# Kernel tuning notes

Hardware: AMD Instinct MI355X
Metric: run time of the kernel (lower is better)

The kernel has to match this reference:

```python
import math
import jax, jax.numpy as jnp
import numpy as np

B, S, HID = 1, 2048, 4096
NH, NKV, HD = 32, 8, 128          # query heads, kv heads, head dim (HID // NH)
G, R = NKV, NH // NKV             # kv groups, query heads per kv group
Q_SIZE, KV_SIZE = NH * HD, NKV * HD


def _get_alibi_slopes(n_heads):
    n = 2 ** math.floor(math.log2(n_heads))
    m0 = 2.0 ** (-8.0 / n)
    slopes = np.power(m0, np.arange(1, n + 1))
    if n < n_heads:
        m1 = 2.0 ** (-4.0 / n)
        mm = np.power(m1, np.arange(1, 1 + 2 * (n_heads - n), 2))
        slopes = np.concatenate([slopes, mm])
    return slopes  # NTK ratio 1.0 -> identity


def setup_inputs() -> dict:
    key = jax.random.key(0)
    k1, k2, k3 = jax.random.split(key, 3)
    positions = jnp.broadcast_to(jnp.arange(S, dtype=jnp.int32), (B, S))
    hidden_states = jax.random.normal(k1, (B, S, HID), dtype=jnp.float32)
    wqkv = jax.random.normal(k2, (Q_SIZE + 2 * KV_SIZE, HID), dtype=jnp.float32) * 0.02
    wo = jax.random.normal(k3, (HID, Q_SIZE), dtype=jnp.float32) * 0.02
    return {"positions": positions, "hidden_states": hidden_states,
            "wqkv": wqkv, "wo": wo}


def reference(positions, hidden_states, wqkv, wo):
    scale = HD ** -0.5
    slopes = jnp.asarray(_get_alibi_slopes(NH), dtype=hidden_states.dtype).reshape(G, R)

    # fused QKV projection (no bias)
    qkv = jnp.einsum('bsh,oh->bso', hidden_states, wqkv)
    q = qkv[..., :Q_SIZE].reshape(B, S, G, R, HD)
    k = qkv[..., Q_SIZE:Q_SIZE + KV_SIZE].reshape(B, S, G, HD)
    v = qkv[..., Q_SIZE + KV_SIZE:].reshape(B, S, G, HD)

    # GQA attention scores: [B, G, R, Sq, Sk]
    scores = jnp.einsum('bqgrd,bkgd->bgrqk', q, k) * scale

    # sqrt-ALiBi bias: -slope * sqrt(q_pos - k_pos), causal mask where k_pos > q_pos
    dist = positions[:, :, None] - positions[:, None, :]            # [B, Sq, Sk]
    bias = -slopes[None, :, :, None, None] * jnp.sqrt(
        jnp.maximum(dist, 0).astype(scores.dtype))[:, None, None]
    neg_inf = jnp.asarray(jnp.finfo(scores.dtype).min, scores.dtype)
    scores = jnp.where(dist[:, None, None] < 0, neg_inf, scores + bias)

    attn = jax.nn.softmax(scores, axis=-1)
    out = jnp.einsum('bgrqk,bkgd->bqgrd', attn, v).reshape(B, S, Q_SIZE)
    return jnp.einsum('bso,ho->bsh', out, wo)
```

## Files before the change

kernel.cpp:

```cpp
#include <hip/hip_runtime.h>
#include <stdint.h>

typedef __attribute__((ext_vector_type(8))) short short8;
typedef __attribute__((ext_vector_type(4))) float floatx4;

#define S_LEN 2048
#define OTOT  6144
#define KOFF  4096
#define VOFF  5120

__device__ __forceinline__ unsigned short f2bf(float f) {
  unsigned int u = __float_as_uint(f);
  u += 0x7FFFu + ((u >> 16) & 1u);
  return (unsigned short)(u >> 16);
}

__device__ __forceinline__ void gload_lds16(const void* g, void* l) {
  __builtin_amdgcn_global_load_lds(
      (const __attribute__((address_space(1))) void*)g,
      (__attribute__((address_space(3))) void*)l, 16, 0, 0);
}

__global__ void cast_bf16_kernel(const float* __restrict__ in,
                                 unsigned short* __restrict__ out, int n4) {
  int i = blockIdx.x * blockDim.x + threadIdx.x;
  int stride = gridDim.x * blockDim.x;
  for (; i < n4; i += stride) {
    float4 v = ((const float4*)in)[i];
    ushort4 o;
    o.x = f2bf(v.x); o.y = f2bf(v.y); o.z = f2bf(v.z); o.w = f2bf(v.w);
    ((ushort4*)out)[i] = o;
  }
}

__global__ void transpose_v_kernel(const unsigned short* __restrict__ qkv,
                                   unsigned short* __restrict__ vt) {
  int tid = blockIdx.x * 256 + threadIdx.x;
  int gd = tid >> 8;
  int s8 = (tid & 255) << 3;
  short8 v;
#pragma unroll
  for (int j = 0; j < 8; ++j)
    v[j] = (short)qkv[(size_t)(s8 + j) * OTOT + VOFF + gd];
  *(short8*)&vt[(size_t)gd * S_LEN + s8] = v;
}

template <typename CT>
__global__ __launch_bounds__(256, 2) void gemm_bt_kernel(
    const unsigned short* __restrict__ A, const unsigned short* __restrict__ B,
    CT* __restrict__ C, int M, int N, int K) {
  __shared__ unsigned short As[128 * 64];
  __shared__ unsigned short Bs[128 * 64];

  int nbn = N >> 7;
  int nwg = gridDim.x;
  int bid = blockIdx.x;
  if ((nwg & 7) == 0) bid = (bid & 7) * (nwg >> 3) + (bid >> 3);
  int bm = bid / nbn, bn = bid % nbn;

  int tid = threadIdx.x;
  int lane = tid & 63, wave = tid >> 6;
  int lr = lane & 15, lh = lane >> 4;
  int wm = (wave >> 1) << 6, wn = (wave & 1) << 6;

  floatx4 acc[4][4];
#pragma unroll
  for (int i = 0; i < 4; ++i)
#pragma unroll
    for (int j = 0; j < 4; ++j) acc[i][j] = (floatx4){0.f, 0.f, 0.f, 0.f};

  const size_t arow = (size_t)bm * 128;
  const size_t brow = (size_t)bn * 128;
  int nk = K >> 6;
  for (int kt = 0; kt < nk; ++kt) {
#pragma unroll
    for (int i = 0; i < 4; ++i) {
      int lin = i * 4096 + tid * 16;
      int row = lin >> 7;
      int colb = (lin & 127) ^ ((row & 7) << 4);
      gload_lds16(&A[(arow + row) * K + kt * 64 + (colb >> 1)],
                  &As[(i * 4096 + wave * 1024) >> 1]);
    }
#pragma unroll
    for (int i = 0; i < 4; ++i) {
      int lin = i * 4096 + tid * 16;
      int row = lin >> 7;
      int colb = (lin & 127) ^ ((row & 7) << 4);
      gload_lds16(&B[(brow + row) * K + kt * 64 + (colb >> 1)],
                  &Bs[(i * 4096 + wave * 1024) >> 1]);
    }
    __syncthreads();
#pragma unroll
    for (int kk = 0; kk < 2; ++kk) {
      short8 af[4], bfr[4];
#pragma unroll
      for (int mi = 0; mi < 4; ++mi) {
        int row = wm + mi * 16 + lr;
        int off = (row << 7) | ((kk * 64 + lh * 16) ^ ((row & 7) << 4));
        af[mi] = *(const short8*)&As[off >> 1];
      }
#pragma unroll
      for (int ni = 0; ni < 4; ++ni) {
        int row = wn + ni * 16 + lr;
        int off = (row << 7) | ((kk * 64 + lh * 16) ^ ((row & 7) << 4));
        bfr[ni] = *(const short8*)&Bs[off >> 1];
      }
#pragma unroll
      for (int mi = 0; mi < 4; ++mi)
#pragma unroll
        for (int ni = 0; ni < 4; ++ni)
          acc[mi][ni] = __builtin_amdgcn_mfma_f32_16x16x32_bf16(
              af[mi], bfr[ni], acc[mi][ni], 0, 0, 0);
    }
    __syncthreads();
  }
#pragma unroll
  for (int mi = 0; mi < 4; ++mi)
#pragma unroll
    for (int ni = 0; ni < 4; ++ni)
#pragma unroll
      for (int r = 0; r < 4; ++r) {
        size_t grow = arow + wm + mi * 16 + lh * 4 + r;
        size_t gcol = brow + wn + ni * 16 + lr;
        float v = acc[mi][ni][r];
        if constexpr (sizeof(CT) == 2)
          ((unsigned short*)C)[grow * N + gcol] = f2bf(v);
        else
          C[grow * N + gcol] = v;
      }
}

__global__ __launch_bounds__(256, 2) void attn_kernel(
    const unsigned short* __restrict__ qkv, const unsigned short* __restrict__ vt,
    const int* __restrict__ pos, unsigned short* __restrict__ aout) {
  __shared__ unsigned short Klds[64 * 128];
  __shared__ unsigned short Vlds[128 * 64];
  __shared__ unsigned short Plds[4][16 * 72];

  int bid = blockIdx.x;
  bid = (bid & 7) * 128 + (bid >> 3);
  int h = bid >> 5, qt = bid & 31;
  int g = h >> 2;
  float slope = exp2f(-0.25f * (float)(h + 1));

  int tid = threadIdx.x, lane = tid & 63, wave = tid >> 6;
  int lr = lane & 15, lh = lane >> 4;
  int qbase = qt * 64;
  int qrow0 = qbase + wave * 16;

  short8 aq[4];
#pragma unroll
  for (int kk = 0; kk < 4; ++kk)
    aq[kk] = *(const short8*)&qkv[(size_t)(qrow0 + lr) * OTOT + h * 128 + kk * 32 + lh * 8];

  int qpos[4];
#pragma unroll
  for (int r = 0; r < 4; ++r) qpos[r] = pos[qrow0 + lh * 4 + r];

  float m_run[4] = {-3.0e38f, -3.0e38f, -3.0e38f, -3.0e38f};
  float l_run[4] = {0.f, 0.f, 0.f, 0.f};
  floatx4 acc_o[8];
#pragma unroll
  for (int n = 0; n < 8; ++n) acc_o[n] = (floatx4){0.f, 0.f, 0.f, 0.f};

  const float scale = 0.08838834764831845f;
  const float LOG2E = 1.4426950408889634f;

  for (int j = 0; j <= qt; ++j) {
    int kbase = j * 64;
#pragma unroll
    for (int i = 0; i < 4; ++i) {
      int lin = i * 4096 + tid * 16;
      int row = lin >> 8;
      int colb = (lin & 255) ^ ((row & 7) << 4);
      gload_lds16(&qkv[(size_t)(kbase + row) * OTOT + KOFF + g * 128 + (colb >> 1)],
                  &Klds[(i * 4096 + wave * 1024) >> 1]);
    }
#pragma unroll
    for (int i = 0; i < 4; ++i) {
      int lin = i * 4096 + tid * 16;
      int row = lin >> 7;
      int colb = (lin & 127) ^ ((row & 7) << 4);
      gload_lds16(&vt[(size_t)(g * 128 + row) * S_LEN + kbase + (colb >> 1)],
                  &Vlds[(i * 4096 + wave * 1024) >> 1]);
    }
    __syncthreads();

    floatx4 sc[4];
#pragma unroll
    for (int n = 0; n < 4; ++n) sc[n] = (floatx4){0.f, 0.f, 0.f, 0.f};
#pragma unroll
    for (int kk = 0; kk < 4; ++kk)
#pragma unroll
      for (int n = 0; n < 4; ++n) {
        int row = n * 16 + lr;
        int off = (row << 8) | ((kk * 64 + lh * 16) ^ ((row & 7) << 4));
        short8 bk = *(const short8*)&Klds[off >> 1];
        sc[n] = __builtin_amdgcn_mfma_f32_16x16x32_bf16(aq[kk], bk, sc[n], 0, 0, 0);
      }

    float p[4][4];
#pragma unroll
    for (int n = 0; n < 4; ++n) {
      int kp = pos[kbase + n * 16 + lr];
#pragma unroll
      for (int r = 0; r < 4; ++r) {
        int dist = qpos[r] - kp;
        p[n][r] = (dist < 0) ? -3.0e38f
                             : sc[n][r] * scale - slope * sqrtf((float)dist);
      }
    }
#pragma unroll
    for (int r = 0; r < 4; ++r) {
      float mx = fmaxf(fmaxf(p[0][r], p[1][r]), fmaxf(p[2][r], p[3][r]));
      mx = fmaxf(mx, __shfl_xor(mx, 1));
      mx = fmaxf(mx, __shfl_xor(mx, 2));
      mx = fmaxf(mx, __shfl_xor(mx, 4));
      mx = fmaxf(mx, __shfl_xor(mx, 8));
      float mnew = fmaxf(m_run[r], mx);
      float rs = 0.f;
#pragma unroll
      for (int n = 0; n < 4; ++n) {
        float e = exp2f((p[n][r] - mnew) * LOG2E);
        p[n][r] = e;
        rs += e;
      }
      rs += __shfl_xor(rs, 1);
      rs += __shfl_xor(rs, 2);
      rs += __shfl_xor(rs, 4);
      rs += __shfl_xor(rs, 8);
      float alpha = exp2f((m_run[r] - mnew) * LOG2E);
      l_run[r] = l_run[r] * alpha + rs;
      m_run[r] = mnew;
#pragma unroll
      for (int n = 0; n < 8; ++n) acc_o[n][r] *= alpha;
    }
#pragma unroll
    for (int n = 0; n < 4; ++n)
#pragma unroll
      for (int r = 0; r < 4; ++r)
        Plds[wave][(lh * 4 + r) * 72 + n * 16 + lr] = f2bf(p[n][r]);

#pragma unroll
    for (int kk = 0; kk < 2; ++kk) {
      short8 pa = *(const short8*)&Plds[wave][lr * 72 + kk * 32 + lh * 8];
#pragma unroll
      for (int n = 0; n < 8; ++n) {
        int row = n * 16 + lr;
        int off = (row << 7) | ((kk * 64 + lh * 16) ^ ((row & 7) << 4));
        short8 bv = *(const short8*)&Vlds[off >> 1];
        acc_o[n] = __builtin_amdgcn_mfma_f32_16x16x32_bf16(pa, bv, acc_o[n], 0, 0, 0);
      }
    }
    __syncthreads();
  }

#pragma unroll
  for (int r = 0; r < 4; ++r) {
    float inv = 1.0f / l_run[r];
    size_t grow = (size_t)(qrow0 + lh * 4 + r);
#pragma unroll
    for (int n = 0; n < 8; ++n)
      aout[grow * 4096 + h * 128 + n * 16 + lr] = f2bf(acc_o[n][r] * inv);
  }
}

extern "C" void kernel_launch(void* const* d_in, const int* in_sizes, int n_in,
                              void* d_out, int out_size, void* d_ws, size_t ws_size,
                              hipStream_t stream) {
  (void)in_sizes; (void)n_in; (void)out_size;
  const int* positions = (const int*)d_in[0];
  const float* hidden = (const float*)d_in[1];
  const float* wqkv = (const float*)d_in[2];
  const float* wo = (const float*)d_in[3];
  float* out = (float*)d_out;

  char* w = (char*)d_ws;
  unsigned short* hbf   = (unsigned short*)(w);
  unsigned short* wqbf  = (unsigned short*)(w + 16777216);
  unsigned short* wobf  = (unsigned short*)(w + 67108864);
  unsigned short* qkv   = (unsigned short*)(w + 100663296);
  unsigned short* vtb   = (unsigned short*)(w + 125829120);
  unsigned short* attnb = (unsigned short*)(w + 130023424);
  if (ws_size < 146800640) return;

  cast_bf16_kernel<<<2048, 256, 0, stream>>>(hidden, hbf, 2048 * 4096 / 4);
  cast_bf16_kernel<<<2048, 256, 0, stream>>>(wqkv, wqbf, 6144 * 4096 / 4);
  cast_bf16_kernel<<<2048, 256, 0, stream>>>(wo, wobf, 4096 * 4096 / 4);

  gemm_bt_kernel<unsigned short><<<768, 256, 0, stream>>>(hbf, wqbf, qkv, 2048, 6144, 4096);
  transpose_v_kernel<<<1024, 256, 0, stream>>>(qkv, vtb);
  attn_kernel<<<1024, 256, 0, stream>>>(qkv, vtb, positions, attnb);
  gemm_bt_kernel<float><<<512, 256, 0, stream>>>(attnb, wobf, out, 2048, 4096, 4096);
}
```

Before: 629.1 us.

## Restructure attention to transposed S^T layout keeping P in registers, tile V transpose

The attention kernel now computes S transposed (K as the A operand, Q as B), so each lane owns one query row. Softmax probabilities can then be packed straight into MFMA operands with v_cvt_pk_bf16_f32, with no LDS round trip, and row reductions need only two cross-lane shuffles. It also adds lazy rescaling, which skips the accumulator update unless the max grows past a threshold. Other changes: pre-scaling by log2e, heaviest query tiles scheduled first, occupancy hint raised to 4, and an LDS-tiled V transpose with coalesced accesses. The risks are register pressure at the higher occupancy target and small numeric drift from the deferred rescale.

```diff
diff --git a/kernel.cpp b/kernel.cpp
--- a/kernel.cpp
+++ b/kernel.cpp
@@ -13,6 +13,12 @@
   unsigned int u = __float_as_uint(f);
   u += 0x7FFFu + ((u >> 16) & 1u);
   return (unsigned short)(u >> 16);
+}
+
+__device__ __forceinline__ unsigned int pack2bf(float lo, float hi) {
+  unsigned int r;
+  asm("v_cvt_pk_bf16_f32 %0, %1, %2" : "=v"(r) : "v"(lo), "v"(hi));
+  return r;
 }
 
 __device__ __forceinline__ void gload_lds16(const void* g, void* l) {
@@ -33,16 +39,30 @@
   }
 }
 
-__global__ void transpose_v_kernel(const unsigned short* __restrict__ qkv,
-                                   unsigned short* __restrict__ vt) {
-  int tid = blockIdx.x * 256 + threadIdx.x;
-  int gd = tid >> 8;
-  int s8 = (tid & 255) << 3;
-  short8 v;
-#pragma unroll
-  for (int j = 0; j < 8; ++j)
-    v[j] = (short)qkv[(size_t)(s8 + j) * OTOT + VOFF + gd];
-  *(short8*)&vt[(size_t)gd * S_LEN + s8] = v;
+__global__ __launch_bounds__(256) void transpose_v_kernel(
+    const unsigned short* __restrict__ qkv, unsigned short* __restrict__ vt) {
+  __shared__ unsigned short T[128 * 74];
+  int s0 = (blockIdx.x & 31) * 64;
+  int g = blockIdx.x >> 5;
+  int tid = threadIdx.x;
+#pragma unroll
+  for (int it = 0; it < 16; ++it) {
+    int idx = it * 256 + tid;
+    int srow = idx >> 6;
+    int dc = idx & 63;
+    unsigned int v = *(const unsigned int*)&qkv[(size_t)(s0 + srow) * OTOT + VOFF + g * 128 + dc * 2];
+    T[(2 * dc) * 74 + srow] = (unsigned short)(v & 0xFFFF);
+    T[(2 * dc + 1) * 74 + srow] = (unsigned short)(v >> 16);
+  }
+  __syncthreads();
+#pragma unroll
+  for (int it = 0; it < 16; ++it) {
+    int odx = it * 256 + tid;
+    int d = odx >> 5;
+    int sc2 = odx & 31;
+    unsigned int w = *(const unsigned int*)&T[d * 74 + 2 * sc2];
+    *(unsigned int*)&vt[(size_t)(g * 128 + d) * S_LEN + s0 + 2 * sc2] = w;
+  }
 }
 
 template <typename CT>
@@ -130,49 +150,44 @@
       }
 }
 
-__global__ __launch_bounds__(256, 2) void attn_kernel(
+__global__ __launch_bounds__(256, 4) void attn_kernel(
     const unsigned short* __restrict__ qkv, const unsigned short* __restrict__ vt,
     const int* __restrict__ pos, unsigned short* __restrict__ aout) {
   __shared__ unsigned short Klds[64 * 128];
   __shared__ unsigned short Vlds[128 * 64];
-  __shared__ unsigned short Plds[4][16 * 72];
 
   int bid = blockIdx.x;
-  bid = (bid & 7) * 128 + (bid >> 3);
-  int h = bid >> 5, qt = bid & 31;
+  int h = bid & 31;
+  int qt = 31 - (bid >> 5);
   int g = h >> 2;
-  float slope = exp2f(-0.25f * (float)(h + 1));
+  const float L2E = 1.4426950408889634f;
+  float slope2 = exp2f(-0.25f * (float)(h + 1)) * L2E;
+  const float QS2 = 0.08838834764831845f * L2E;
+  const float THR = 8.0f * L2E;
 
   int tid = threadIdx.x, lane = tid & 63, wave = tid >> 6;
   int lr = lane & 15, lh = lane >> 4;
-  int qbase = qt * 64;
-  int qrow0 = qbase + wave * 16;
-
-  short8 aq[4];
+  int qrow0 = qt * 64 + wave * 16;
+
+  short8 qf[4];
 #pragma unroll
   for (int kk = 0; kk < 4; ++kk)
-    aq[kk] = *(const short8*)&qkv[(size_t)(qrow0 + lr) * OTOT + h * 128 + kk * 32 + lh * 8];
-
-  int qpos[4];
-#pragma unroll
-  for (int r = 0; r < 4; ++r) qpos[r] = pos[qrow0 + lh * 4 + r];
-
-  float m_run[4] = {-3.0e38f, -3.0e38f, -3.0e38f, -3.0e38f};
-  float l_run[4] = {0.f, 0.f, 0.f, 0.f};
-  floatx4 acc_o[8];
-#pragma unroll
-  for (int n = 0; n < 8; ++n) acc_o[n] = (floatx4){0.f, 0.f, 0.f, 0.f};
-
-  const float scale = 0.08838834764831845f;
-  const float LOG2E = 1.4426950408889634f;
-
-  for (int j = 0; j <= qt; ++j) {
+    qf[kk] = *(const short8*)&qkv[(size_t)(qrow0 + lr) * OTOT + h * 128 + kk * 32 + lh * 8];
+  int qpos = pos[qrow0 + lr];
+
+  float m_run = -3.0e38f, l_run = 0.f;
+  floatx4 acc[8];
+#pragma unroll
+  for (int n = 0; n < 8; ++n) acc[n] = (floatx4){0.f, 0.f, 0.f, 0.f};
+
+  for (int jj = 0; jj <= qt; ++jj) {
+    int j = qt - jj;
     int kbase = j * 64;
 #pragma unroll
     for (int i = 0; i < 4; ++i) {
       int lin = i * 4096 + tid * 16;
       int row = lin >> 8;
-      int colb = (lin & 255) ^ ((row & 7) << 4);
+      int colb = (lin & 255) ^ (((row >> 1) & 7) << 4);
       gload_lds16(&qkv[(size_t)(kbase + row) * OTOT + KOFF + g * 128 + (colb >> 1)],
                   &Klds[(i * 4096 + wave * 1024) >> 1]);
     }
@@ -190,78 +205,88 @@
 #pragma unroll
     for (int n = 0; n < 4; ++n) sc[n] = (floatx4){0.f, 0.f, 0.f, 0.f};
 #pragma unroll
-    for (int kk = 0; kk < 4; ++kk)
-#pragma unroll
-      for (int n = 0; n < 4; ++n) {
-        int row = n * 16 + lr;
-        int off = (row << 8) | ((kk * 64 + lh * 16) ^ ((row & 7) << 4));
-        short8 bk = *(const short8*)&Klds[off >> 1];
-        sc[n] = __builtin_amdgcn_mfma_f32_16x16x32_bf16(aq[kk], bk, sc[n], 0, 0, 0);
-      }
-
-    float p[4][4];
-#pragma unroll
     for (int n = 0; n < 4; ++n) {
-      int kp = pos[kbase + n * 16 + lr];
+      int rowk = 32 * (n & 1) + 2 * lr + (n >> 1);
+      int swz = ((rowk >> 1) & 7) << 4;
+#pragma unroll
+      for (int kk = 0; kk < 4; ++kk) {
+        short8 kf = *(const short8*)&Klds[((rowk << 8) | ((kk * 64 + lh * 16) ^ swz)) >> 1];
+        sc[n] = __builtin_amdgcn_mfma_f32_16x16x32_bf16(kf, qf[kk], sc[n], 0, 0, 0);
+      }
+    }
+
+    int4 a0 = *(const int4*)&pos[kbase + lh * 8];
+    int4 a1 = *(const int4*)&pos[kbase + lh * 8 + 4];
+    int4 b0 = *(const int4*)&pos[kbase + 32 + lh * 8];
+    int4 b1 = *(const int4*)&pos[kbase + 32 + lh * 8 + 4];
+    int klo[8] = {a0.x, a0.y, a0.z, a0.w, a1.x, a1.y, a1.z, a1.w};
+    int khi[8] = {b0.x, b0.y, b0.z, b0.w, b1.x, b1.y, b1.z, b1.w};
+
+#pragma unroll
+    for (int n = 0; n < 4; ++n)
 #pragma unroll
       for (int r = 0; r < 4; ++r) {
-        int dist = qpos[r] - kp;
-        p[n][r] = (dist < 0) ? -3.0e38f
-                             : sc[n][r] * scale - slope * sqrtf((float)dist);
-      }
-    }
-#pragma unroll
-    for (int r = 0; r < 4; ++r) {
-      float mx = fmaxf(fmaxf(p[0][r], p[1][r]), fmaxf(p[2][r], p[3][r]));
-      mx = fmaxf(mx, __shfl_xor(mx, 1));
-      mx = fmaxf(mx, __shfl_xor(mx, 2));
-      mx = fmaxf(mx, __shfl_xor(mx, 4));
-      mx = fmaxf(mx, __shfl_xor(mx, 8));
-      float mnew = fmaxf(m_run[r], mx);
-      float rs = 0.f;
-#pragma unroll
-      for (int n = 0; n < 4; ++n) {
-        float e = exp2f((p[n][r] - mnew) * LOG2E);
-        p[n][r] = e;
-        rs += e;
-      }
-      rs += __shfl_xor(rs, 1);
-      rs += __shfl_xor(rs, 2);
-      rs += __shfl_xor(rs, 4);
-      rs += __shfl_xor(rs, 8);
-      float alpha = exp2f((m_run[r] - mnew) * LOG2E);
-      l_run[r] = l_run[r] * alpha + rs;
-      m_run[r] = mnew;
-#pragma unroll
-      for (int n = 0; n < 8; ++n) acc_o[n][r] *= alpha;
-    }
+        int jidx = 2 * r + (n >> 1);
+        int kp = (n & 1) ? khi[jidx] : klo[jidx];
+        int dist = qpos - kp;
+        float sv = sc[n][r] * QS2 - slope2 * sqrtf((float)dist);
+        sc[n][r] = (dist < 0) ? -1.0e38f : sv;
+      }
+
+    float mx = sc[0][0];
 #pragma unroll
     for (int n = 0; n < 4; ++n)
 #pragma unroll
-      for (int r = 0; r < 4; ++r)
-        Plds[wave][(lh * 4 + r) * 72 + n * 16 + lr] = f2bf(p[n][r]);
-
-#pragma unroll
-    for (int kk = 0; kk < 2; ++kk) {
-      short8 pa = *(const short8*)&Plds[wave][lr * 72 + kk * 32 + lh * 8];
-#pragma unroll
-      for (int n = 0; n < 8; ++n) {
-        int row = n * 16 + lr;
-        int off = (row << 7) | ((kk * 64 + lh * 16) ^ ((row & 7) << 4));
-        short8 bv = *(const short8*)&Vlds[off >> 1];
-        acc_o[n] = __builtin_amdgcn_mfma_f32_16x16x32_bf16(pa, bv, acc_o[n], 0, 0, 0);
-      }
+      for (int r = 0; r < 4; ++r) mx = fmaxf(mx, sc[n][r]);
+    mx = fmaxf(mx, __shfl_xor(mx, 16));
+    mx = fmaxf(mx, __shfl_xor(mx, 32));
+
+    if (__any(mx > m_run + THR)) {
+      float mnew = fmaxf(m_run, mx);
+      float al = exp2f(m_run - mnew);
+      l_run *= al;
+#pragma unroll
+      for (int n = 0; n < 8; ++n) acc[n] *= al;
+      m_run = mnew;
+    }
+
+    float rs = 0.f;
+    union { unsigned int u[4]; short8 v; } pf0, pf1;
+#pragma unroll
+    for (int w = 0; w < 4; ++w) {
+      float e0 = exp2f(sc[0][w] - m_run);
+      float e2 = exp2f(sc[2][w] - m_run);
+      float e1 = exp2f(sc[1][w] - m_run);
+      float e3 = exp2f(sc[3][w] - m_run);
+      rs += (e0 + e2) + (e1 + e3);
+      pf0.u[w] = pack2bf(e0, e2);
+      pf1.u[w] = pack2bf(e1, e3);
+    }
+    rs += __shfl_xor(rs, 16);
+    rs += __shfl_xor(rs, 32);
+    l_run += rs;
+
+#pragma unroll
+    for (int n = 0; n < 8; ++n) {
+      int rowv = n * 16 + lr;
+      int swz = (rowv & 7) << 4;
+      short8 v0 = *(const short8*)&Vlds[((rowv << 7) | ((lh * 16) ^ swz)) >> 1];
+      short8 v1 = *(const short8*)&Vlds[((rowv << 7) | ((64 + lh * 16) ^ swz)) >> 1];
+      acc[n] = __builtin_amdgcn_mfma_f32_16x16x32_bf16(v0, pf0.v, acc[n], 0, 0, 0);
+      acc[n] = __builtin_amdgcn_mfma_f32_16x16x32_bf16(v1, pf1.v, acc[n], 0, 0, 0);
     }
     __syncthreads();
   }
 
-#pragma unroll
-  for (int r = 0; r < 4; ++r) {
-    float inv = 1.0f / l_run[r];
-    size_t grow = (size_t)(qrow0 + lh * 4 + r);
-#pragma unroll
-    for (int n = 0; n < 8; ++n)
-      aout[grow * 4096 + h * 128 + n * 16 + lr] = f2bf(acc_o[n][r] * inv);
+  float inv = 1.0f / l_run;
+#pragma unroll
+  for (int n = 0; n < 8; ++n) {
+    ushort4 o;
+    o.x = f2bf(acc[n][0] * inv);
+    o.y = f2bf(acc[n][1] * inv);
+    o.z = f2bf(acc[n][2] * inv);
+    o.w = f2bf(acc[n][3] * inv);
+    *(ushort4*)&aout[(size_t)(qrow0 + lr) * 4096 + h * 128 + n * 16 + lh * 4] = o;
   }
 }
 
@@ -289,7 +314,7 @@
   cast_bf16_kernel<<<2048, 256, 0, stream>>>(wo, wobf, 4096 * 4096 / 4);
 
   gemm_bt_kernel<unsigned short><<<768, 256, 0, stream>>>(hbf, wqbf, qkv, 2048, 6144, 4096);
-  transpose_v_kernel<<<1024, 256, 0, stream>>>(qkv, vtb);
+  transpose_v_kernel<<<256, 256, 0, stream>>>(qkv, vtb);
   attn_kernel<<<1024, 256, 0, stream>>>(qkv, vtb, positions, attnb);
   gemm_bt_kernel<float><<<512, 256, 0, stream>>>(attnb, wobf, out, 2048, 4096, 4096);
 }
```

After: 519.0 us. -17.5%, faster.
